# Optimization experiments

Hardware: AMD Instinct MI355X
Metric: run time of the kernel (lower is better)

The kernel has to match this reference:

```python
import jax, jax.numpy as jnp
import numpy as np

N, E = 50000, 600000
D_IN, D_H, D_OUT = 128, 128, 128


def sage_conv(x, src, dst, w_l, b_l, w_r, num_nodes):
    """PyG SAGEConv with mean aggregation: lin_l(mean_j x_j) + lin_r(x_i).
    lin_l has bias, lin_r has no bias (PyG defaults)."""
    msgs = x[src]                                                    # [E, d] gather
    agg = jax.ops.segment_sum(msgs, dst, num_segments=num_nodes)    # [N, d] scatter-add
    deg = jax.ops.segment_sum(jnp.ones((src.shape[0],), x.dtype), dst,
                              num_segments=num_nodes)               # [N]
    agg = agg / jnp.maximum(deg, 1.0)[:, None]                      # mean
    return agg @ w_l + b_l + x @ w_r


def setup_inputs() -> dict:
    key = jax.random.key(0)
    ks = jax.random.split(key, 7)
    s = 1.0 / np.sqrt(D_IN)
    return {
        "x": jax.random.normal(ks[0], (N, D_IN), dtype=jnp.float32),
        "edge_index": jax.random.randint(ks[1], (2, E), 0, N, dtype=jnp.int64),
        "w_l1": jax.random.normal(ks[2], (D_IN, D_H), dtype=jnp.float32) * s,
        "b_l1": jnp.zeros((D_H,), dtype=jnp.float32),
        "w_r1": jax.random.normal(ks[3], (D_IN, D_H), dtype=jnp.float32) * s,
        "w_l2": jax.random.normal(ks[4], (D_H, D_OUT), dtype=jnp.float32) * s,
        "b_l2": jnp.zeros((D_OUT,), dtype=jnp.float32),
        "w_r2": jax.random.normal(ks[5], (D_H, D_OUT), dtype=jnp.float32) * s,
    }


def reference(x, edge_index, w_l1, b_l1, w_r1, w_l2, b_l2, w_r2):
    src, dst = edge_index[0], edge_index[1]
    num_nodes = x.shape[0]
    h = sage_conv(x, src, dst, w_l1, b_l1, w_r1, num_nodes)
    h = jax.nn.relu(h)
    # F.dropout with training=False is the identity (inference reference)
    out = sage_conv(h, src, dst, w_l2, b_l2, w_r2, num_nodes)
    return out
```

## Files before the change

### kernel.cpp

```cpp
#include <hip/hip_runtime.h>
#include <hip/hip_bf16.h>


#define D 128
#define PAD 64

typedef __attribute__((ext_vector_type(8))) short bf16x8;
typedef __attribute__((ext_vector_type(4))) float f32x4;

__device__ __forceinline__ unsigned short f2bf(float f) {
    __hip_bfloat16 b = __float2bfloat16(f);
    return *(unsigned short*)&b;
}
__device__ __forceinline__ float bf_lo(unsigned u) { return __uint_as_float(u << 16); }
__device__ __forceinline__ float bf_hi(unsigned u) { return __uint_as_float(u & 0xffff0000u); }

__global__ __launch_bounds__(256) void prep_kernel(
    const float* __restrict__ x, unsigned short* __restrict__ xb, int n4,
    const float* __restrict__ w0, const float* __restrict__ w1,
    const float* __restrict__ w2, const float* __restrict__ w3,
    unsigned short* __restrict__ o0, unsigned short* __restrict__ o1,
    unsigned short* __restrict__ o2, unsigned short* __restrict__ o3,
    int* __restrict__ cursor, int n, int nb_f2bf) {
    int b = blockIdx.x;
    int tid = threadIdx.x;
    if (b < nb_f2bf) {
        int i = b * 256 + tid;
        if (i < n4) {
            float4 v = ((const float4*)x)[i];
            ushort4 o;
            o.x = f2bf(v.x); o.y = f2bf(v.y); o.z = f2bf(v.z); o.w = f2bf(v.w);
            ((ushort4*)xb)[i] = o;
        }
    } else if (b < nb_f2bf + 256) {
        int t = (b - nb_f2bf) * 256 + tid;
        int m = t >> 14;
        int r = t & 16383;
        int f = r >> 9;
        int q = r & 511;
        int lane = q >> 3, j = q & 7;
        int kt = f & 3, c = f >> 2;
        int k  = kt * 32 + (lane >> 4) * 8 + j;
        int nn = c * 16 + (lane & 15);
        const float* w = (m == 0) ? w0 : (m == 1) ? w1 : (m == 2) ? w2 : w3;
        unsigned short* o = (m == 0) ? o0 : (m == 1) ? o1 : (m == 2) ? o2 : o3;
        o[r] = f2bf(w[k * 128 + nn]);
    } else {
        int i = (b - nb_f2bf - 256) * 256 + tid;
        if (i < n) cursor[i] = 0;
    }
}

__global__ void fill_pad_kernel(const int* __restrict__ src, const int* __restrict__ dst,
                                int* __restrict__ cursor, int* __restrict__ csr, int E) {
    int i = blockIdx.x * blockDim.x + threadIdx.x;
    if (i < E) {
        int d = dst[i];
        int p = atomicAdd(&cursor[d], 1);
        if (p < PAD) csr[d * PAD + p] = src[i];
    }
}

__global__ __launch_bounds__(256) void aggregate_bf16_kernel(
    const unsigned short* __restrict__ feat, const int* __restrict__ deg,
    const int* __restrict__ csr, unsigned short* __restrict__ agg, int n) {
    int gw = (blockIdx.x * 256 + threadIdx.x) >> 6;
    int lane = threadIdx.x & 63;
    if (gw >= n) return;
    const int g = lane >> 4;
    const int s = lane & 15;
    int beg = gw * PAD;
    int cnt = deg[gw];
    if (cnt > PAD) cnt = PAD;

    float a0 = 0.f, a1 = 0.f, a2 = 0.f, a3 = 0.f;
    float a4 = 0.f, a5 = 0.f, a6 = 0.f, a7 = 0.f;
    float b0 = 0.f, b1 = 0.f, b2 = 0.f, b3 = 0.f;
    float b4 = 0.f, b5 = 0.f, b6 = 0.f, b7 = 0.f;

    int j = 0;
    for (; j + 8 <= cnt; j += 8) {
        int nA = csr[beg + j + g];
        int nB = csr[beg + j + 4 + g];
        uint4 uA = *(const uint4*)(feat + (size_t)nA * D + s * 8);
        uint4 uB = *(const uint4*)(feat + (size_t)nB * D + s * 8);
        a0 += bf_lo(uA.x); a1 += bf_hi(uA.x);
        a2 += bf_lo(uA.y); a3 += bf_hi(uA.y);
        a4 += bf_lo(uA.z); a5 += bf_hi(uA.z);
        a6 += bf_lo(uA.w); a7 += bf_hi(uA.w);
        b0 += bf_lo(uB.x); b1 += bf_hi(uB.x);
        b2 += bf_lo(uB.y); b3 += bf_hi(uB.y);
        b4 += bf_lo(uB.z); b5 += bf_hi(uB.z);
        b6 += bf_lo(uB.w); b7 += bf_hi(uB.w);
    }
    if (j + 4 <= cnt) {
        int nA = csr[beg + j + g];
        uint4 uA = *(const uint4*)(feat + (size_t)nA * D + s * 8);
        a0 += bf_lo(uA.x); a1 += bf_hi(uA.x);
        a2 += bf_lo(uA.y); a3 += bf_hi(uA.y);
        a4 += bf_lo(uA.z); a5 += bf_hi(uA.z);
        a6 += bf_lo(uA.w); a7 += bf_hi(uA.w);
        j += 4;
    }
    int rem = cnt - j;
    if (g < rem) {
        int nA = csr[beg + j + g];
        uint4 uA = *(const uint4*)(feat + (size_t)nA * D + s * 8);
        b0 += bf_lo(uA.x); b1 += bf_hi(uA.x);
        b2 += bf_lo(uA.y); b3 += bf_hi(uA.y);
        b4 += bf_lo(uA.z); b5 += bf_hi(uA.z);
        b6 += bf_lo(uA.w); b7 += bf_hi(uA.w);
    }
    a0 += b0; a1 += b1; a2 += b2; a3 += b3;
    a4 += b4; a5 += b5; a6 += b6; a7 += b7;

    a0 += __shfl_xor(a0, 16, 64); a0 += __shfl_xor(a0, 32, 64);
    a1 += __shfl_xor(a1, 16, 64); a1 += __shfl_xor(a1, 32, 64);
    a2 += __shfl_xor(a2, 16, 64); a2 += __shfl_xor(a2, 32, 64);
    a3 += __shfl_xor(a3, 16, 64); a3 += __shfl_xor(a3, 32, 64);
    a4 += __shfl_xor(a4, 16, 64); a4 += __shfl_xor(a4, 32, 64);
    a5 += __shfl_xor(a5, 16, 64); a5 += __shfl_xor(a5, 32, 64);
    a6 += __shfl_xor(a6, 16, 64); a6 += __shfl_xor(a6, 32, 64);
    a7 += __shfl_xor(a7, 16, 64); a7 += __shfl_xor(a7, 32, 64);

    if (g == 0) {
        float sc = 1.0f / (float)(cnt > 0 ? cnt : 1);
        uint4 o;
        o.x = ((unsigned)f2bf(a1 * sc) << 16) | (unsigned)f2bf(a0 * sc);
        o.y = ((unsigned)f2bf(a3 * sc) << 16) | (unsigned)f2bf(a2 * sc);
        o.z = ((unsigned)f2bf(a5 * sc) << 16) | (unsigned)f2bf(a4 * sc);
        o.w = ((unsigned)f2bf(a7 * sc) << 16) | (unsigned)f2bf(a6 * sc);
        *(uint4*)(agg + (size_t)gw * D + s * 8) = o;
    }
}

__global__ __launch_bounds__(256) void gemm_mfma_kernel(
    const unsigned short* __restrict__ A, const unsigned short* __restrict__ X,
    const unsigned short* __restrict__ WfL, const unsigned short* __restrict__ WfR,
    const float* __restrict__ bias, unsigned short* __restrict__ out_bf,
    float* __restrict__ out_f32, int n, int mode, int ntiles) {
    __shared__ unsigned short lds[2][32][512];

    const int tid = threadIdx.x;
    {
        const uint4* srcL = (const uint4*)WfL;
        const uint4* srcR = (const uint4*)WfR;
        uint4* dst = (uint4*)&lds[0][0][0];
#pragma unroll
        for (int it = 0; it < 8; ++it) {
            int i = it * 256 + tid;
            dst[i]        = srcL[i];
            dst[2048 + i] = srcR[i];
        }
    }
    __syncthreads();

    const int wid = tid >> 6;
    const int lane = tid & 63;
    const int quad = lane >> 4;
    const int l16 = lane & 15;

    for (int tile = blockIdx.x; tile < ntiles; tile += gridDim.x) {
        const int row0 = tile * 64 + wid * 16;
        int m = row0 + l16;
        if (m >= n) m = n - 1;

        bf16x8 af[2][4];
        const unsigned short* apA = A + (size_t)m * D + quad * 8;
        const unsigned short* apX = X + (size_t)m * D + quad * 8;
#pragma unroll
        for (int kt = 0; kt < 4; ++kt) {
            af[0][kt] = *(const bf16x8*)(apA + kt * 32);
            af[1][kt] = *(const bf16x8*)(apX + kt * 32);
        }

        f32x4 acc[8];
#pragma unroll
        for (int c = 0; c < 8; ++c) acc[c] = (f32x4){0.f, 0.f, 0.f, 0.f};

#pragma unroll
        for (int half = 0; half < 2; ++half) {
#pragma unroll
            for (int kt = 0; kt < 4; ++kt) {
#pragma unroll
                for (int c = 0; c < 8; ++c) {
                    bf16x8 bfrag = *(const bf16x8*)&lds[half][c * 4 + kt][lane * 8];
                    acc[c] = __builtin_amdgcn_mfma_f32_16x16x32_bf16(af[half][kt], bfrag, acc[c], 0, 0, 0);
                }
            }
        }

#pragma unroll
        for (int c = 0; c < 8; ++c) {
            int col = c * 16 + l16;
            float bb = bias[col];
#pragma unroll
            for (int r = 0; r < 4; ++r) {
                int row = row0 + quad * 4 + r;
                if (row < n) {
                    float v = acc[c][r] + bb;
                    if (mode) {
                        v = fmaxf(v, 0.0f);
                        out_bf[(size_t)row * D + col] = f2bf(v);
                    } else {
                        out_f32[(size_t)row * D + col] = v;
                    }
                }
            }
        }
    }
}


extern "C" void kernel_launch(void* const* d_in, const int* in_sizes, int n_in,
                              void* d_out, int out_size, void* d_ws, size_t ws_size,
                              hipStream_t stream) {
    const float* x   = (const float*)d_in[0];
    const int*   edg = (const int*)d_in[1];
    const float* wl1 = (const float*)d_in[2];
    const float* bl1 = (const float*)d_in[3];
    const float* wr1 = (const float*)d_in[4];
    const float* wl2 = (const float*)d_in[5];
    const float* bl2 = (const float*)d_in[6];
    const float* wr2 = (const float*)d_in[7];
    float* out = (float*)d_out;

    const int N = in_sizes[0] / D;
    const int E = in_sizes[1] / 2;
    const int* src = edg;
    const int* dst = edg + E;
    const int NB = (N + 255) / 256;

    char* ws = (char*)d_ws;
    size_t off = 0;
    auto carve = [&](size_t bytes) -> char* {
        char* p = ws + off;
        off = (off + bytes + 255) & ~(size_t)255;
        return p;
    };
    int*   cursor  = (int*)  carve((size_t)N * 4);
    int*   csr     = (int*)  carve((size_t)N * PAD * 4);
    unsigned short* xb   = (unsigned short*)carve((size_t)N * D * 2);
    unsigned short* hb   = (unsigned short*)carve((size_t)N * D * 2);
    unsigned short* aggb = (unsigned short*)carve((size_t)N * D * 2);
    unsigned short* wtl1 = (unsigned short*)carve(16384 * 2);
    unsigned short* wtr1 = (unsigned short*)carve(16384 * 2);
    unsigned short* wtl2 = (unsigned short*)carve(16384 * 2);
    unsigned short* wtr2 = (unsigned short*)carve(16384 * 2);
    (void)ws_size;

    int n4 = N * D / 4;
    int nb_f2bf = (n4 + 255) / 256;
    int prep_blocks = nb_f2bf + 256 + NB;

    prep_kernel<<<prep_blocks, 256, 0, stream>>>(
        x, xb, n4, wl1, wr1, wl2, wr2, wtl1, wtr1, wtl2, wtr2, cursor, N, nb_f2bf);

    int eb = (E + 255) / 256;
    fill_pad_kernel<<<eb, 256, 0, stream>>>(src, dst, cursor, csr, E);

    int agg_blocks = (N + 3) / 4;
    int ntiles = (N + 63) / 64;
    int gemm_blocks = (ntiles + 1) / 2;

    aggregate_bf16_kernel<<<agg_blocks, 256, 0, stream>>>(xb, cursor, csr, aggb, N);
    gemm_mfma_kernel<<<gemm_blocks, 256, 0, stream>>>(aggb, xb, wtl1, wtr1, bl1, hb, (float*)nullptr, N, 1, ntiles);

    aggregate_bf16_kernel<<<agg_blocks, 256, 0, stream>>>(hb, cursor, csr, aggb, N);
    gemm_mfma_kernel<<<gemm_blocks, 256, 0, stream>>>(aggb, hb, wtl2, wtr2, bl2, (unsigned short*)nullptr, out, N, 0, ntiles);
}
```

Baseline: 210.9 us.

## Fuse mean aggregation into the MFMA GEMM via LDS staging

Replaces the separate aggregate and GEMM kernels with one kernel per layer. Each block gathers and averages neighbour features for its 64 rows into a swizzled LDS tile, then runs the MFMA GEMM reading the aggregated A fragments from LDS. This removes the global write and re-read of the aggregated buffer and two launches. In exchange, LDS use per block grows, lowering occupancy, and each wave aggregates 16 rows serially, which may hurt latency hiding of the gathers; weights are reloaded per 64-row tile.

```diff
diff --git a/kernel.cpp b/kernel.cpp
--- a/kernel.cpp
+++ b/kernel.cpp
@@ -61,150 +61,150 @@
     }
 }
 
-__global__ __launch_bounds__(256) void aggregate_bf16_kernel(
-    const unsigned short* __restrict__ feat, const int* __restrict__ deg,
-    const int* __restrict__ csr, unsigned short* __restrict__ agg, int n) {
-    int gw = (blockIdx.x * 256 + threadIdx.x) >> 6;
-    int lane = threadIdx.x & 63;
-    if (gw >= n) return;
-    const int g = lane >> 4;
-    const int s = lane & 15;
-    int beg = gw * PAD;
-    int cnt = deg[gw];
-    if (cnt > PAD) cnt = PAD;
-
-    float a0 = 0.f, a1 = 0.f, a2 = 0.f, a3 = 0.f;
-    float a4 = 0.f, a5 = 0.f, a6 = 0.f, a7 = 0.f;
-    float b0 = 0.f, b1 = 0.f, b2 = 0.f, b3 = 0.f;
-    float b4 = 0.f, b5 = 0.f, b6 = 0.f, b7 = 0.f;
-
-    int j = 0;
-    for (; j + 8 <= cnt; j += 8) {
-        int nA = csr[beg + j + g];
-        int nB = csr[beg + j + 4 + g];
-        uint4 uA = *(const uint4*)(feat + (size_t)nA * D + s * 8);
-        uint4 uB = *(const uint4*)(feat + (size_t)nB * D + s * 8);
-        a0 += bf_lo(uA.x); a1 += bf_hi(uA.x);
-        a2 += bf_lo(uA.y); a3 += bf_hi(uA.y);
-        a4 += bf_lo(uA.z); a5 += bf_hi(uA.z);
-        a6 += bf_lo(uA.w); a7 += bf_hi(uA.w);
-        b0 += bf_lo(uB.x); b1 += bf_hi(uB.x);
-        b2 += bf_lo(uB.y); b3 += bf_hi(uB.y);
-        b4 += bf_lo(uB.z); b5 += bf_hi(uB.z);
-        b6 += bf_lo(uB.w); b7 += bf_hi(uB.w);
-    }
-    if (j + 4 <= cnt) {
-        int nA = csr[beg + j + g];
-        uint4 uA = *(const uint4*)(feat + (size_t)nA * D + s * 8);
-        a0 += bf_lo(uA.x); a1 += bf_hi(uA.x);
-        a2 += bf_lo(uA.y); a3 += bf_hi(uA.y);
-        a4 += bf_lo(uA.z); a5 += bf_hi(uA.z);
-        a6 += bf_lo(uA.w); a7 += bf_hi(uA.w);
-        j += 4;
-    }
-    int rem = cnt - j;
-    if (g < rem) {
-        int nA = csr[beg + j + g];
-        uint4 uA = *(const uint4*)(feat + (size_t)nA * D + s * 8);
-        b0 += bf_lo(uA.x); b1 += bf_hi(uA.x);
-        b2 += bf_lo(uA.y); b3 += bf_hi(uA.y);
-        b4 += bf_lo(uA.z); b5 += bf_hi(uA.z);
-        b6 += bf_lo(uA.w); b7 += bf_hi(uA.w);
-    }
-    a0 += b0; a1 += b1; a2 += b2; a3 += b3;
-    a4 += b4; a5 += b5; a6 += b6; a7 += b7;
-
-    a0 += __shfl_xor(a0, 16, 64); a0 += __shfl_xor(a0, 32, 64);
-    a1 += __shfl_xor(a1, 16, 64); a1 += __shfl_xor(a1, 32, 64);
-    a2 += __shfl_xor(a2, 16, 64); a2 += __shfl_xor(a2, 32, 64);
-    a3 += __shfl_xor(a3, 16, 64); a3 += __shfl_xor(a3, 32, 64);
-    a4 += __shfl_xor(a4, 16, 64); a4 += __shfl_xor(a4, 32, 64);
-    a5 += __shfl_xor(a5, 16, 64); a5 += __shfl_xor(a5, 32, 64);
-    a6 += __shfl_xor(a6, 16, 64); a6 += __shfl_xor(a6, 32, 64);
-    a7 += __shfl_xor(a7, 16, 64); a7 += __shfl_xor(a7, 32, 64);
-
-    if (g == 0) {
-        float sc = 1.0f / (float)(cnt > 0 ? cnt : 1);
-        uint4 o;
-        o.x = ((unsigned)f2bf(a1 * sc) << 16) | (unsigned)f2bf(a0 * sc);
-        o.y = ((unsigned)f2bf(a3 * sc) << 16) | (unsigned)f2bf(a2 * sc);
-        o.z = ((unsigned)f2bf(a5 * sc) << 16) | (unsigned)f2bf(a4 * sc);
-        o.w = ((unsigned)f2bf(a7 * sc) << 16) | (unsigned)f2bf(a6 * sc);
-        *(uint4*)(agg + (size_t)gw * D + s * 8) = o;
-    }
-}
-
-__global__ __launch_bounds__(256) void gemm_mfma_kernel(
-    const unsigned short* __restrict__ A, const unsigned short* __restrict__ X,
+__global__ __launch_bounds__(256) void fused_agg_gemm_kernel(
+    const unsigned short* __restrict__ feat,
     const unsigned short* __restrict__ WfL, const unsigned short* __restrict__ WfR,
+    const int* __restrict__ deg, const int* __restrict__ csr,
     const float* __restrict__ bias, unsigned short* __restrict__ out_bf,
-    float* __restrict__ out_f32, int n, int mode, int ntiles) {
-    __shared__ unsigned short lds[2][32][512];
+    float* __restrict__ out_f32, int n, int mode) {
+    __shared__ unsigned short ldsw[2][32][512];
+    __shared__ unsigned short ldsa[64][128];
 
     const int tid = threadIdx.x;
     {
         const uint4* srcL = (const uint4*)WfL;
         const uint4* srcR = (const uint4*)WfR;
-        uint4* dst = (uint4*)&lds[0][0][0];
+        uint4* dstw = (uint4*)&ldsw[0][0][0];
 #pragma unroll
         for (int it = 0; it < 8; ++it) {
             int i = it * 256 + tid;
-            dst[i]        = srcL[i];
-            dst[2048 + i] = srcR[i];
+            dstw[i]        = srcL[i];
+            dstw[2048 + i] = srcR[i];
+        }
+    }
+
+    const int wid  = tid >> 6;
+    const int lane = tid & 63;
+    const int g = lane >> 4;
+    const int s = lane & 15;
+    const int row0 = blockIdx.x * 64;
+
+    for (int i = 0; i < 16; ++i) {
+        const int r = wid * 16 + i;
+        const int m = row0 + r;
+
+        float a0 = 0.f, a1 = 0.f, a2 = 0.f, a3 = 0.f;
+        float a4 = 0.f, a5 = 0.f, a6 = 0.f, a7 = 0.f;
+        int cnt = 0;
+        if (m < n) {
+            cnt = deg[m];
+            if (cnt > PAD) cnt = PAD;
+            int beg = m * PAD;
+            float b0 = 0.f, b1 = 0.f, b2 = 0.f, b3 = 0.f;
+            float b4 = 0.f, b5 = 0.f, b6 = 0.f, b7 = 0.f;
+            int j = 0;
+            for (; j + 8 <= cnt; j += 8) {
+                int nA = csr[beg + j + g];
+                int nB = csr[beg + j + 4 + g];
+                uint4 uA = *(const uint4*)(feat + (size_t)nA * D + s * 8);
+                uint4 uB = *(const uint4*)(feat + (size_t)nB * D + s * 8);
+                a0 += bf_lo(uA.x); a1 += bf_hi(uA.x);
+                a2 += bf_lo(uA.y); a3 += bf_hi(uA.y);
+                a4 += bf_lo(uA.z); a5 += bf_hi(uA.z);
+                a6 += bf_lo(uA.w); a7 += bf_hi(uA.w);
+                b0 += bf_lo(uB.x); b1 += bf_hi(uB.x);
+                b2 += bf_lo(uB.y); b3 += bf_hi(uB.y);
+                b4 += bf_lo(uB.z); b5 += bf_hi(uB.z);
+                b6 += bf_lo(uB.w); b7 += bf_hi(uB.w);
+            }
+            if (j + 4 <= cnt) {
+                int nA = csr[beg + j + g];
+                uint4 uA = *(const uint4*)(feat + (size_t)nA * D + s * 8);
+                a0 += bf_lo(uA.x); a1 += bf_hi(uA.x);
+                a2 += bf_lo(uA.y); a3 += bf_hi(uA.y);
+                a4 += bf_lo(uA.z); a5 += bf_hi(uA.z);
+                a6 += bf_lo(uA.w); a7 += bf_hi(uA.w);
+                j += 4;
+            }
+            int rem = cnt - j;
+            if (g < rem) {
+                int nA = csr[beg + j + g];
+                uint4 uA = *(const uint4*)(feat + (size_t)nA * D + s * 8);
+                b0 += bf_lo(uA.x); b1 += bf_hi(uA.x);
+                b2 += bf_lo(uA.y); b3 += bf_hi(uA.y);
+                b4 += bf_lo(uA.z); b5 += bf_hi(uA.z);
+                b6 += bf_lo(uA.w); b7 += bf_hi(uA.w);
+            }
+            a0 += b0; a1 += b1; a2 += b2; a3 += b3;
+            a4 += b4; a5 += b5; a6 += b6; a7 += b7;
+        }
+
+        a0 += __shfl_xor(a0, 16, 64); a0 += __shfl_xor(a0, 32, 64);
+        a1 += __shfl_xor(a1, 16, 64); a1 += __shfl_xor(a1, 32, 64);
+        a2 += __shfl_xor(a2, 16, 64); a2 += __shfl_xor(a2, 32, 64);
+        a3 += __shfl_xor(a3, 16, 64); a3 += __shfl_xor(a3, 32, 64);
+        a4 += __shfl_xor(a4, 16, 64); a4 += __shfl_xor(a4, 32, 64);
+        a5 += __shfl_xor(a5, 16, 64); a5 += __shfl_xor(a5, 32, 64);
+        a6 += __shfl_xor(a6, 16, 64); a6 += __shfl_xor(a6, 32, 64);
+        a7 += __shfl_xor(a7, 16, 64); a7 += __shfl_xor(a7, 32, 64);
+
+        if (g == 0) {
+            float sc = 1.0f / (float)(cnt > 0 ? cnt : 1);
+            uint4 o;
+            o.x = ((unsigned)f2bf(a1 * sc) << 16) | (unsigned)f2bf(a0 * sc);
+            o.y = ((unsigned)f2bf(a3 * sc) << 16) | (unsigned)f2bf(a2 * sc);
+            o.z = ((unsigned)f2bf(a5 * sc) << 16) | (unsigned)f2bf(a4 * sc);
+            o.w = ((unsigned)f2bf(a7 * sc) << 16) | (unsigned)f2bf(a6 * sc);
+            *(uint4*)&ldsa[r][(s ^ (r & 15)) * 8] = o;
         }
     }
     __syncthreads();
 
-    const int wid = tid >> 6;
-    const int lane = tid & 63;
     const int quad = lane >> 4;
-    const int l16 = lane & 15;
-
-    for (int tile = blockIdx.x; tile < ntiles; tile += gridDim.x) {
-        const int row0 = tile * 64 + wid * 16;
-        int m = row0 + l16;
-        if (m >= n) m = n - 1;
-
-        bf16x8 af[2][4];
-        const unsigned short* apA = A + (size_t)m * D + quad * 8;
-        const unsigned short* apX = X + (size_t)m * D + quad * 8;
+    const int l16  = lane & 15;
+    const int rloc = wid * 16 + l16;
+    int mc = row0 + rloc;
+    if (mc >= n) mc = n - 1;
+
+    bf16x8 af[2][4];
+    const unsigned short* apX = feat + (size_t)mc * D + quad * 8;
+#pragma unroll
+    for (int kt = 0; kt < 4; ++kt) {
+        int c = kt * 4 + quad;
+        af[0][kt] = *(const bf16x8*)&ldsa[rloc][(c ^ (rloc & 15)) * 8];
+        af[1][kt] = *(const bf16x8*)(apX + kt * 32);
+    }
+
+    f32x4 acc[8];
+#pragma unroll
+    for (int c = 0; c < 8; ++c) acc[c] = (f32x4){0.f, 0.f, 0.f, 0.f};
+
+#pragma unroll
+    for (int half = 0; half < 2; ++half) {
 #pragma unroll
         for (int kt = 0; kt < 4; ++kt) {
-            af[0][kt] = *(const bf16x8*)(apA + kt * 32);
-            af[1][kt] = *(const bf16x8*)(apX + kt * 32);
-        }
-
-        f32x4 acc[8];
-#pragma unroll
-        for (int c = 0; c < 8; ++c) acc[c] = (f32x4){0.f, 0.f, 0.f, 0.f};
-
-#pragma unroll
-        for (int half = 0; half < 2; ++half) {
-#pragma unroll
-            for (int kt = 0; kt < 4; ++kt) {
-#pragma unroll
-                for (int c = 0; c < 8; ++c) {
-                    bf16x8 bfrag = *(const bf16x8*)&lds[half][c * 4 + kt][lane * 8];
-                    acc[c] = __builtin_amdgcn_mfma_f32_16x16x32_bf16(af[half][kt], bfrag, acc[c], 0, 0, 0);
-                }
-            }
-        }
-
-#pragma unroll
-        for (int c = 0; c < 8; ++c) {
-            int col = c * 16 + l16;
-            float bb = bias[col];
-#pragma unroll
-            for (int r = 0; r < 4; ++r) {
-                int row = row0 + quad * 4 + r;
-                if (row < n) {
-                    float v = acc[c][r] + bb;
-                    if (mode) {
-                        v = fmaxf(v, 0.0f);
-                        out_bf[(size_t)row * D + col] = f2bf(v);
-                    } else {
-                        out_f32[(size_t)row * D + col] = v;
-                    }
+#pragma unroll
+            for (int c = 0; c < 8; ++c) {
+                bf16x8 bfrag = *(const bf16x8*)&ldsw[half][c * 4 + kt][lane * 8];
+                acc[c] = __builtin_amdgcn_mfma_f32_16x16x32_bf16(af[half][kt], bfrag, acc[c], 0, 0, 0);
+            }
+        }
+    }
+
+#pragma unroll
+    for (int c = 0; c < 8; ++c) {
+        int col = c * 16 + l16;
+        float bb = bias[col];
+#pragma unroll
+        for (int r = 0; r < 4; ++r) {
+            int row = row0 + wid * 16 + quad * 4 + r;
+            if (row < n) {
+                float v = acc[c][r] + bb;
+                if (mode) {
+                    v = fmaxf(v, 0.0f);
+                    out_bf[(size_t)row * D + col] = f2bf(v);
+                } else {
+                    out_f32[(size_t)row * D + col] = v;
                 }
             }
         }
@@ -242,7 +242,6 @@
     int*   csr     = (int*)  carve((size_t)N * PAD * 4);
     unsigned short* xb   = (unsigned short*)carve((size_t)N * D * 2);
     unsigned short* hb   = (unsigned short*)carve((size_t)N * D * 2);
-    unsigned short* aggb = (unsigned short*)carve((size_t)N * D * 2);
     unsigned short* wtl1 = (unsigned short*)carve(16384 * 2);
     unsigned short* wtr1 = (unsigned short*)carve(16384 * 2);
     unsigned short* wtl2 = (unsigned short*)carve(16384 * 2);
@@ -259,13 +258,11 @@
     int eb = (E + 255) / 256;
     fill_pad_kernel<<<eb, 256, 0, stream>>>(src, dst, cursor, csr, E);
 
-    int agg_blocks = (N + 3) / 4;
     int ntiles = (N + 63) / 64;
-    int gemm_blocks = (ntiles + 1) / 2;
-
-    aggregate_bf16_kernel<<<agg_blocks, 256, 0, stream>>>(xb, cursor, csr, aggb, N);
-    gemm_mfma_kernel<<<gemm_blocks, 256, 0, stream>>>(aggb, xb, wtl1, wtr1, bl1, hb, (float*)nullptr, N, 1, ntiles);
-
-    aggregate_bf16_kernel<<<agg_blocks, 256, 0, stream>>>(hb, cursor, csr, aggb, N);
-    gemm_mfma_kernel<<<gemm_blocks, 256, 0, stream>>>(aggb, hb, wtl2, wtr2, bl2, (unsigned short*)nullptr, out, N, 0, ntiles);
-}
+
+    fused_agg_gemm_kernel<<<ntiles, 256, 0, stream>>>(
+        xb, wtl1, wtr1, cursor, csr, bl1, hb, (float*)nullptr, N, 1);
+
+    fused_agg_gemm_kernel<<<ntiles, 256, 0, stream>>>(
+        hb, wtl2, wtr2, cursor, csr, bl2, (unsigned short*)nullptr, out, N, 0);
+}
```

Result: slower. 292.1 us (+38.5%).
